# Performance work log

Hardware: AMD Instinct MI355X
Metric: run time of the kernel (lower is better)

Reference implementation:

```python
import jax, jax.numpy as jnp
import numpy as np

EMBED = 768
HIDDEN = 3072
HEADS = 12
EPS = 1e-6


def _ln(x, g, b):
    mu = jnp.mean(x, axis=-1, keepdims=True)
    var = jnp.mean(jnp.square(x - mu), axis=-1, keepdims=True)
    return (x - mu) / jnp.sqrt(var + EPS) * g + b


def setup_inputs() -> dict:
    key = jax.random.key(0)
    ks = jax.random.split(key, 12)
    s = lambda fan_in: 1.0 / np.sqrt(fan_in)
    x = jax.random.normal(ks[0], (16, 1024, EMBED), dtype=jnp.float32)
    return {
        "x": x,
        "ln1_g": jnp.ones((EMBED,), jnp.float32),
        "ln1_b": jnp.zeros((EMBED,), jnp.float32),
        "qkv_w": jax.random.uniform(ks[1], (3 * EMBED, EMBED), jnp.float32, -s(EMBED), s(EMBED)),
        "qkv_b": jax.random.uniform(ks[2], (3 * EMBED,), jnp.float32, -s(EMBED), s(EMBED)),
        "proj_w": jax.random.uniform(ks[3], (EMBED, EMBED), jnp.float32, -s(EMBED), s(EMBED)),
        "proj_b": jax.random.uniform(ks[4], (EMBED,), jnp.float32, -s(EMBED), s(EMBED)),
        "ln2_g": jnp.ones((EMBED,), jnp.float32),
        "ln2_b": jnp.zeros((EMBED,), jnp.float32),
        "fc1_w": jax.random.uniform(ks[5], (HIDDEN, EMBED), jnp.float32, -s(EMBED), s(EMBED)),
        "fc1_b": jax.random.uniform(ks[6], (HIDDEN,), jnp.float32, -s(EMBED), s(EMBED)),
        "fc2_w": jax.random.uniform(ks[7], (EMBED, HIDDEN), jnp.float32, -s(HIDDEN), s(HIDDEN)),
        "fc2_b": jax.random.uniform(ks[8], (EMBED,), jnp.float32, -s(HIDDEN), s(HIDDEN)),
    }


def reference(x, ln1_g, ln1_b, qkv_w, qkv_b, proj_w, proj_b, ln2_g, ln2_b, fc1_w, fc1_b, fc2_w, fc2_b):
    B, N, D = x.shape
    Hd = D // HEADS
    scale = Hd ** -0.5
    # attention branch
    xn = _ln(x, ln1_g, ln1_b)
    qkv = xn @ qkv_w.T + qkv_b  # [B,N,3D]
    qkv = qkv.reshape(B, N, 3, HEADS, Hd).transpose(2, 0, 3, 1, 4)
    q, k, v = qkv[0], qkv[1], qkv[2]  # [B,H,N,Hd]
    attn = jax.nn.softmax(jnp.einsum("bhqd,bhkd->bhqk", q, k) * scale, axis=-1)
    ctx = jnp.einsum("bhqk,bhkd->bhqd", attn, v)
    ctx = ctx.transpose(0, 2, 1, 3).reshape(B, N, D)
    x = x + ctx @ proj_w.T + proj_b
    # MLP branch
    h = _ln(x, ln2_g, ln2_b)
    h = jax.nn.gelu(h @ fc1_w.T + fc1_b, approximate=False)
    x = x + h @ fc2_w.T + fc2_b
    return x
```

## Files before the change

### kernel.cpp

```cpp
#include <hip/hip_runtime.h>
#include <math.h>


typedef unsigned short u16;
typedef __attribute__((ext_vector_type(8))) short bf16x8;
typedef __attribute__((ext_vector_type(4))) float f32x4;

#define MFMA_BF16(a, b, c) __builtin_amdgcn_mfma_f32_16x16x32_bf16((a), (b), (c), 0, 0, 0)
#define MEMFENCE asm volatile("" ::: "memory")
#define WAITV(N) asm volatile("s_waitcnt vmcnt(" #N ")" ::: "memory")
#define WAITLGKM0 asm volatile("s_waitcnt lgkmcnt(0)" ::: "memory")
#define SCHED0 __builtin_amdgcn_sched_barrier(0)

__device__ __forceinline__ float bf2f(u16 v) {
    return __uint_as_float(((unsigned)v) << 16);
}
__device__ __forceinline__ u16 f2bf(float f) {
    unsigned u = __float_as_uint(f);
    u += 0x7fffu + ((u >> 16) & 1u);
    return (u16)(u >> 16);
}

__device__ __forceinline__ float gelu_fast(float v) {
    const float t = v * v;
    const float z = v * (1.5957691216f + 0.0713548162f * t);
    const float e = __expf(-z);
    return v * __builtin_amdgcn_rcpf(1.0f + e);
}

typedef __attribute__((address_space(1))) const void gvoid;
typedef __attribute__((address_space(3))) void lvoid;
__device__ __forceinline__ void gll16(const void* g, void* l) {
    __builtin_amdgcn_global_load_lds((gvoid*)g, (lvoid*)l, 16, 0, 0);
}

__global__ __launch_bounds__(256) void cast32(const float* __restrict__ src,
                                              u16* __restrict__ dst, int n8) {
    const int i = blockIdx.x * 256 + threadIdx.x;
    if (i >= n8) return;
    const float4 a = ((const float4*)src)[2 * i];
    const float4 b = ((const float4*)src)[2 * i + 1];
    bf16x8 r;
    r[0] = (short)f2bf(a.x); r[1] = (short)f2bf(a.y);
    r[2] = (short)f2bf(a.z); r[3] = (short)f2bf(a.w);
    r[4] = (short)f2bf(b.x); r[5] = (short)f2bf(b.y);
    r[6] = (short)f2bf(b.z); r[7] = (short)f2bf(b.w);
    ((bf16x8*)dst)[i] = r;
}

__global__ __launch_bounds__(256) void ln_kernel(const float* __restrict__ x,
                                                 const float* __restrict__ g,
                                                 const float* __restrict__ b,
                                                 u16* __restrict__ out) {
    const int row = blockIdx.x;
    const int t = threadIdx.x;
    const float* xr = x + (size_t)row * 768;
    float v0 = xr[t], v1 = xr[t + 256], v2 = xr[t + 512];
    float s = v0 + v1 + v2;
    float sq = v0 * v0 + v1 * v1 + v2 * v2;
#pragma unroll
    for (int off = 32; off > 0; off >>= 1) {
        s += __shfl_down(s, off);
        sq += __shfl_down(sq, off);
    }
    __shared__ float red_s[4], red_sq[4], sh_mu, sh_rs;
    const int wave = t >> 6, lane = t & 63;
    if (lane == 0) { red_s[wave] = s; red_sq[wave] = sq; }
    __syncthreads();
    if (t == 0) {
        float S = red_s[0] + red_s[1] + red_s[2] + red_s[3];
        float SQ = red_sq[0] + red_sq[1] + red_sq[2] + red_sq[3];
        float mu = S * (1.0f / 768.0f);
        float var = SQ * (1.0f / 768.0f) - mu * mu;
        sh_mu = mu;
        sh_rs = 1.0f / sqrtf(fmaxf(var, 0.0f) + 1e-6f);
    }
    __syncthreads();
    const float mu = sh_mu, rs = sh_rs;
    u16* orow = out + (size_t)row * 768;
    orow[t]       = f2bf((v0 - mu) * rs * g[t]       + b[t]);
    orow[t + 256] = f2bf((v1 - mu) * rs * g[t + 256] + b[t + 256]);
    orow[t + 512] = f2bf((v2 - mu) * rs * g[t + 512] + b[t + 512]);
}

template <int EPI, int BF16B>
__global__ __launch_bounds__(256, 2) void gemm2(
        const u16* __restrict__ A, const void* __restrict__ Bv,
        const float* __restrict__ bias, const float* __restrict__ res,
        void* __restrict__ Cv, u16* __restrict__ vtb, int N, int K) {
    __shared__ __align__(16) u16 As[128 * 32];
    __shared__ __align__(16) u16 Bs[128 * 32];
    const int t = threadIdx.x;
    const int wave = t >> 6, lane = t & 63;
    const int quad = lane >> 4, mr = lane & 15;
    const int wm = wave >> 1, wn = wave & 1;
    const int m0 = blockIdx.y * 128;
    const int n0 = blockIdx.x * 128;

    f32x4 acc[4][4];
#pragma unroll
    for (int i = 0; i < 4; i++)
#pragma unroll
        for (int j = 0; j < 4; j++) acc[i][j] = (f32x4){0.f, 0.f, 0.f, 0.f};

    const int seg = wave * 2;
    const int drow = lane >> 2;
    const int dcol = (lane & 3) * 8;
    const int sr = t >> 2, skv = t & 3;

    for (int k0 = 0; k0 < K; k0 += 32) {
#pragma unroll
        for (int c = 0; c < 2; c++) {
            const int rowA = (seg + c) * 16 + drow;
            gll16(A + (size_t)(m0 + rowA) * K + k0 + dcol, &As[(seg + c) * 512]);
        }
        if (BF16B) {
            const u16* Bh = (const u16*)Bv;
#pragma unroll
            for (int c = 0; c < 2; c++) {
                const int rowB = (seg + c) * 16 + drow;
                gll16(Bh + (size_t)(n0 + rowB) * K + k0 + dcol, &Bs[(seg + c) * 512]);
            }
        } else {
            const float* Bf = (const float*)Bv;
#pragma unroll
            for (int half = 0; half < 2; half++) {
                const float* src = Bf + (size_t)(n0 + sr + half * 64) * K + k0 + skv * 8;
                const float4 a = *(const float4*)src;
                const float4 b2 = *(const float4*)(src + 4);
                bf16x8 r;
                r[0] = (short)f2bf(a.x);  r[1] = (short)f2bf(a.y);
                r[2] = (short)f2bf(a.z);  r[3] = (short)f2bf(a.w);
                r[4] = (short)f2bf(b2.x); r[5] = (short)f2bf(b2.y);
                r[6] = (short)f2bf(b2.z); r[7] = (short)f2bf(b2.w);
                *(bf16x8*)&Bs[(sr + half * 64) * 32 + skv * 8] = r;
            }
        }
        __syncthreads();
        bf16x8 af[4], bfr[4];
#pragma unroll
        for (int i = 0; i < 4; i++)
            af[i] = *(const bf16x8*)&As[(wm * 64 + i * 16 + mr) * 32 + quad * 8];
#pragma unroll
        for (int j = 0; j < 4; j++)
            bfr[j] = *(const bf16x8*)&Bs[(wn * 64 + j * 16 + mr) * 32 + quad * 8];
#pragma unroll
        for (int i = 0; i < 4; i++)
#pragma unroll
            for (int j = 0; j < 4; j++)
                acc[i][j] = MFMA_BF16(af[i], bfr[j], acc[i][j]);
        __syncthreads();
    }

#pragma unroll
    for (int i = 0; i < 4; i++) {
#pragma unroll
        for (int r = 0; r < 4; r++) {
            const int m = m0 + wm * 64 + i * 16 + quad * 4 + r;
#pragma unroll
            for (int j = 0; j < 4; j++) {
                const int n = n0 + wn * 64 + j * 16 + mr;
                float v = acc[i][j][r] + bias[n];
                if (EPI == 1) {
                    v = gelu_fast(v);
                    ((u16*)Cv)[(size_t)m * N + n] = f2bf(v);
                } else if (EPI == 2) {
                    v += res[(size_t)m * N + n];
                    ((float*)Cv)[(size_t)m * N + n] = v;
                } else {
                    if (n < 1536) {
                        const float vq = (n < 768) ? v * 0.125f : v;
                        ((u16*)Cv)[(size_t)m * 1536 + n] = f2bf(vq);
                    } else {
                        const int h = (n - 1536) >> 6, hd = (n - 1536) & 63;
                        const int bb = m >> 10, pos = m & 1023;
                        vtb[((size_t)(bb * 12 + h) * 64 + hd) * 1024 + pos] = f2bf(v);
                    }
                }
            }
        }
    }
}

#define AFRAG(T, ROW, KS) \
    (*(const bf16x8*)&(T)[(ROW)][(((((KS) << 2) | quad)) ^ ((ROW) & 7)) << 3])

template <int EPI>
__global__ __launch_bounds__(512, 2) void gemm8(
        const u16* __restrict__ A, const u16* __restrict__ Bw,
        const float* __restrict__ bias, const float* __restrict__ res,
        void* __restrict__ Cv, u16* __restrict__ vtb, int N, int K) {
    __shared__ __align__(16) u16 SMEM[4][256][64];
    u16(&As)[2][256][64] = *reinterpret_cast<u16(*)[2][256][64]>(&SMEM[0][0][0]);
    u16(&Bs)[2][256][64] = *reinterpret_cast<u16(*)[2][256][64]>(&SMEM[2][0][0]);
    const int t = threadIdx.x;
    const int wave = t >> 6, lane = t & 63;
    const int quad = lane >> 4, mr = lane & 15;
    const int wm = wave >> 2, wn = wave & 3;
    const int gx = gridDim.x;
    const int nwg = gx * gridDim.y;
    int bid = blockIdx.y * gx + blockIdx.x;
    bid = (bid & 7) * (nwg >> 3) + (bid >> 3);
    const int m0 = (bid / gx) * 256, n0 = (bid % gx) * 256;
    const int NT = K >> 6;

    const int srow = wave * 8 + (lane >> 3);
    const int sgrp = ((lane & 7) ^ (lane >> 3)) * 8;

    const u16* Abase = A + (size_t)(m0 + srow) * K + sgrp;
    const u16* Bbase = Bw + (size_t)(n0 + srow) * K + sgrp;

#define STAGE_A(BI, SLOT, KT) \
    gll16(Abase + ((size_t)(SLOT) * 64) * K + (KT) * 64, &As[BI][(SLOT) * 64 + wave * 8][0])
#define STAGE_B(BI, SLOT, KT) \
    gll16(Bbase + ((size_t)(SLOT) * 64) * K + (KT) * 64, &Bs[BI][(SLOT) * 64 + wave * 8][0])

    STAGE_A(0, 0, 0); STAGE_A(0, 2, 0);
    STAGE_B(0, 0, 0); STAGE_B(0, 1, 0);
    STAGE_B(0, 2, 0); STAGE_B(0, 3, 0);
    STAGE_A(0, 1, 0); STAGE_A(0, 3, 0);
    if (NT > 1) { STAGE_A(1, 0, 1); STAGE_A(1, 2, 1); STAGE_B(1, 0, 1); STAGE_B(1, 1, 1); }

    f32x4 acc[8][4];
#pragma unroll
    for (int i = 0; i < 8; i++)
#pragma unroll
        for (int j = 0; j < 4; j++) acc[i][j] = (f32x4){0.f, 0.f, 0.f, 0.f};

    if (NT > 1) { WAITV(6); } else { WAITV(2); }
    __builtin_amdgcn_s_barrier();
    SCHED0;

    for (int kt = 0; kt < NT; ++kt) {
        const int bi = kt & 1;
        const u16(*Ab)[64] = As[bi];
        const u16(*Bb)[64] = Bs[bi];
        const bool st1 = (kt + 1 < NT);
        const bool st2 = (kt + 2 < NT);
        bf16x8 af[4], bfv[4];

#pragma unroll
        for (int i = 0; i < 4; i++) af[i] = AFRAG(Ab, wm * 128 + i * 16 + mr, 0);
#pragma unroll
        for (int j = 0; j < 4; j++) bfv[j] = AFRAG(Bb, wn * 64 + j * 16 + mr, 0);
        if (st1) { STAGE_B(bi ^ 1, 2, kt + 1); STAGE_B(bi ^ 1, 3, kt + 1); }
        SCHED0;
        __builtin_amdgcn_s_barrier();
        WAITLGKM0;
        SCHED0;
        __builtin_amdgcn_s_setprio(1);
#pragma unroll
        for (int i = 0; i < 4; i++)
#pragma unroll
            for (int j = 0; j < 4; j++)
                acc[i][j] = MFMA_BF16(af[i], bfv[j], acc[i][j]);
        __builtin_amdgcn_s_setprio(0);
        SCHED0;
        if (st1) { WAITV(6); } else { WAITV(0); }
        __builtin_amdgcn_s_barrier();
        SCHED0;

#pragma unroll
        for (int i = 0; i < 4; i++) af[i] = AFRAG(Ab, wm * 128 + 64 + i * 16 + mr, 0);
        if (st1) { STAGE_A(bi ^ 1, 1, kt + 1); STAGE_A(bi ^ 1, 3, kt + 1); }
        SCHED0;
        __builtin_amdgcn_s_barrier();
        WAITLGKM0;
        SCHED0;
        __builtin_amdgcn_s_setprio(1);
#pragma unroll
        for (int i = 0; i < 4; i++)
#pragma unroll
            for (int j = 0; j < 4; j++)
                acc[4 + i][j] = MFMA_BF16(af[i], bfv[j], acc[4 + i][j]);
        __builtin_amdgcn_s_setprio(0);
        SCHED0;
        __builtin_amdgcn_s_barrier();
        SCHED0;

#pragma unroll
        for (int i = 0; i < 4; i++) af[i] = AFRAG(Ab, wm * 128 + i * 16 + mr, 1);
#pragma unroll
        for (int j = 0; j < 4; j++) bfv[j] = AFRAG(Bb, wn * 64 + j * 16 + mr, 1);
        SCHED0;
        __builtin_amdgcn_s_barrier();
        WAITLGKM0;
        SCHED0;
        __builtin_amdgcn_s_setprio(1);
#pragma unroll
        for (int i = 0; i < 4; i++)
#pragma unroll
            for (int j = 0; j < 4; j++)
                acc[i][j] = MFMA_BF16(af[i], bfv[j], acc[i][j]);
        __builtin_amdgcn_s_setprio(0);
        SCHED0;
        __builtin_amdgcn_s_barrier();
        SCHED0;

#pragma unroll
        for (int i = 0; i < 4; i++) af[i] = AFRAG(Ab, wm * 128 + 64 + i * 16 + mr, 1);
        if (st2) { STAGE_A(bi, 0, kt + 2); STAGE_A(bi, 2, kt + 2);
                   STAGE_B(bi, 0, kt + 2); STAGE_B(bi, 1, kt + 2); }
        SCHED0;
        __builtin_amdgcn_s_barrier();
        WAITLGKM0;
        SCHED0;
        __builtin_amdgcn_s_setprio(1);
#pragma unroll
        for (int i = 0; i < 4; i++)
#pragma unroll
            for (int j = 0; j < 4; j++)
                acc[4 + i][j] = MFMA_BF16(af[i], bfv[j], acc[4 + i][j]);
        __builtin_amdgcn_s_setprio(0);
        SCHED0;
        if (st2) { WAITV(6); } else if (st1) { WAITV(2); }
        __builtin_amdgcn_s_barrier();
        SCHED0;
    }

    if (EPI == 3 && n0 >= 1536) {
        u16* Ls = &SMEM[0][0][0];
        __syncthreads();
#pragma unroll
        for (int i = 0; i < 8; i++) {
            const int mbase = wm * 128 + i * 16 + quad * 4;
            const int mch = mbase >> 3, mlo = mbase & 7;
#pragma unroll
            for (int j = 0; j < 4; j++) {
                const int nl = wn * 64 + j * 16 + mr;
                float v0 = acc[i][j][0] + bias[n0 + nl];
                float v1 = acc[i][j][1] + bias[n0 + nl];
                float v2 = acc[i][j][2] + bias[n0 + nl];
                float v3 = acc[i][j][3] + bias[n0 + nl];
                ushort4 w;
                w.x = f2bf(v0); w.y = f2bf(v1); w.z = f2bf(v2); w.w = f2bf(v3);
                *(ushort4*)(Ls + nl * 256 + ((mch ^ (nl & 7)) << 3) + mlo) = w;
            }
        }
        __syncthreads();
        const int bb = m0 >> 10, pos0 = m0 & 1023;
#pragma unroll
        for (int it = 0; it < 32; it++) {
            const int nl = it * 8 + wave;
            const int h = (n0 - 1536 + nl) >> 6;
            const int hd = nl & 63;
            const int mch = (lane >> 1) ^ (nl & 7);
            const ushort4 v =
                *(const ushort4*)(Ls + nl * 256 + (mch << 3) + (lane & 1) * 4);
            u16* dst = vtb + ((size_t)(bb * 12 + h) * 64 + hd) * 1024 + pos0 + lane * 4;
            *(ushort4*)dst = v;
        }
    } else {
#pragma unroll
        for (int i = 0; i < 8; i++) {
#pragma unroll
            for (int r = 0; r < 4; r++) {
                const int m = m0 + wm * 128 + i * 16 + quad * 4 + r;
#pragma unroll
                for (int j = 0; j < 4; j++) {
                    const int n = n0 + wn * 64 + j * 16 + mr;
                    float v = acc[i][j][r] + bias[n];
                    if (EPI == 1) {
                        v = gelu_fast(v);
                        ((u16*)Cv)[(size_t)m * N + n] = f2bf(v);
                    } else if (EPI == 2) {
                        v += res[(size_t)m * N + n];
                        ((float*)Cv)[(size_t)m * N + n] = v;
                    } else {
                        const float vq = (n < 768) ? v * 0.125f : v;
                        ((u16*)Cv)[(size_t)m * 1536 + n] = f2bf(vq);
                    }
                }
            }
        }
    }
#undef STAGE_A
#undef STAGE_B
}

__global__ __launch_bounds__(256) void attn2(const u16* __restrict__ qkkb,
                                             const u16* __restrict__ vtb,
                                             u16* __restrict__ ctx) {
    __shared__ __align__(16) u16 Ks[2][64][72];
    __shared__ __align__(16) u16 Vt[2][64][72];
    __shared__ __align__(16) u16 Ps[64][72];
    const int bh = blockIdx.y;
    const int b = bh / 12, h = bh % 12;
    const int q0 = blockIdx.x * 64;
    const int t = threadIdx.x;
    const int wave = t >> 6, lane = t & 63, quad = lane >> 4, mr = lane & 15;

    const u16* qrow = qkkb + (size_t)(b * 1024 + q0 + wave * 16 + mr) * 1536 + h * 64;
    const bf16x8 qf0 = *(const bf16x8*)(qrow + quad * 8);
    const bf16x8 qf1 = *(const bf16x8*)(qrow + 32 + quad * 8);

    const u16* kbase = qkkb + (size_t)b * 1024 * 1536 + 768 + h * 64;
    const u16* vbase = vtb + (size_t)bh * 64 * 1024;

    const int srow = t >> 3;
    const int sv = t & 7;

    f32x4 oacc[4];
#pragma unroll
    for (int j = 0; j < 4; j++) oacc[j] = (f32x4){0.f, 0.f, 0.f, 0.f};
    float lsum[4] = {0.f, 0.f, 0.f, 0.f};

    bf16x8 pk0, pk1, pv0, pv1;
    pk0 = *(const bf16x8*)(kbase + (size_t)(srow)      * 1536 + sv * 8);
    pk1 = *(const bf16x8*)(kbase + (size_t)(srow + 32) * 1536 + sv * 8);
    pv0 = *(const bf16x8*)(vbase + (size_t)(srow)      * 1024 + sv * 8);
    pv1 = *(const bf16x8*)(vbase + (size_t)(srow + 32) * 1024 + sv * 8);
    *(bf16x8*)&Ks[0][srow][sv * 8] = pk0;
    *(bf16x8*)&Ks[0][srow + 32][sv * 8] = pk1;
    *(bf16x8*)&Vt[0][srow][sv * 8] = pv0;
    *(bf16x8*)&Vt[0][srow + 32][sv * 8] = pv1;

    for (int kt = 0; kt < 16; ++kt) {
        __syncthreads();
        const int cur = kt & 1;
        if (kt < 15) {
            const size_t ko = (size_t)(kt + 1) * 64;
            pk0 = *(const bf16x8*)(kbase + (ko + srow)      * 1536 + sv * 8);
            pk1 = *(const bf16x8*)(kbase + (ko + srow + 32) * 1536 + sv * 8);
            pv0 = *(const bf16x8*)(vbase + (size_t)(srow)      * 1024 + ko + sv * 8);
            pv1 = *(const bf16x8*)(vbase + (size_t)(srow + 32) * 1024 + ko + sv * 8);
        }
        f32x4 sf[4];
#pragma unroll
        for (int j = 0; j < 4; j++) {
            const bf16x8 kf0 = *(const bf16x8*)&Ks[cur][j * 16 + mr][quad * 8];
            const bf16x8 kf1 = *(const bf16x8*)&Ks[cur][j * 16 + mr][32 + quad * 8];
            f32x4 s = (f32x4){0.f, 0.f, 0.f, 0.f};
            s = MFMA_BF16(qf0, kf0, s);
            s = MFMA_BF16(qf1, kf1, s);
            sf[j] = s;
        }
#pragma unroll
        for (int r = 0; r < 4; r++) {
            const float p0 = __expf(sf[0][r] - 8.0f);
            const float p1 = __expf(sf[1][r] - 8.0f);
            const float p2 = __expf(sf[2][r] - 8.0f);
            const float p3 = __expf(sf[3][r] - 8.0f);
            lsum[r] += (p0 + p1) + (p2 + p3);
            const int prow = wave * 16 + quad * 4 + r;
            Ps[prow][0 * 16 + mr] = f2bf(p0);
            Ps[prow][1 * 16 + mr] = f2bf(p1);
            Ps[prow][2 * 16 + mr] = f2bf(p2);
            Ps[prow][3 * 16 + mr] = f2bf(p3);
        }
        __asm__ __volatile__("s_waitcnt lgkmcnt(0)" ::: "memory");
#pragma unroll
        for (int st = 0; st < 2; st++) {
            const bf16x8 pf = *(const bf16x8*)&Ps[wave * 16 + mr][st * 32 + quad * 8];
#pragma unroll
            for (int j = 0; j < 4; j++) {
                const bf16x8 vf = *(const bf16x8*)&Vt[cur][j * 16 + mr][st * 32 + quad * 8];
                oacc[j] = MFMA_BF16(pf, vf, oacc[j]);
            }
        }
        if (kt < 15) {
            const int nxt = cur ^ 1;
            *(bf16x8*)&Ks[nxt][srow][sv * 8] = pk0;
            *(bf16x8*)&Ks[nxt][srow + 32][sv * 8] = pk1;
            *(bf16x8*)&Vt[nxt][srow][sv * 8] = pv0;
            *(bf16x8*)&Vt[nxt][srow + 32][sv * 8] = pv1;
        }
    }

#pragma unroll
    for (int r = 0; r < 4; r++) {
#pragma unroll
        for (int off = 1; off < 16; off <<= 1) lsum[r] += __shfl_xor(lsum[r], off);
        const float inv = 1.0f / lsum[r];
        u16* dst = ctx + (size_t)(b * 1024 + q0 + wave * 16 + quad * 4 + r) * 768 + h * 64;
#pragma unroll
        for (int j = 0; j < 4; j++) dst[j * 16 + mr] = f2bf(oacc[j][r] * inv);
    }
}

extern "C" void kernel_launch(void* const* d_in, const int* in_sizes, int n_in,
                              void* d_out, int out_size, void* d_ws, size_t ws_size,
                              hipStream_t stream) {
    const float* x      = (const float*)d_in[0];
    const float* ln1_g  = (const float*)d_in[1];
    const float* ln1_b  = (const float*)d_in[2];
    const float* qkv_w  = (const float*)d_in[3];
    const float* qkv_b  = (const float*)d_in[4];
    const float* proj_w = (const float*)d_in[5];
    const float* proj_b = (const float*)d_in[6];
    const float* ln2_g  = (const float*)d_in[7];
    const float* ln2_b  = (const float*)d_in[8];
    const float* fc1_w  = (const float*)d_in[9];
    const float* fc1_b  = (const float*)d_in[10];
    const float* fc2_w  = (const float*)d_in[11];
    const float* fc2_b  = (const float*)d_in[12];
    float* out = (float*)d_out;

    char* base = (char*)d_ws + 1024;
    u16* xn   = (u16*)base;
    u16* qkkb = (u16*)(base + 25165824);
    u16* vtb  = (u16*)(base + 75497472);
    u16* h1   = (u16*)(base + 25165824);
    u16* ctxb = xn;
    u16* hn   = xn;

    const size_t WOFF = 125830144ull;
    const bool big = ws_size >= 139985920ull;
    u16* wqkv  = (u16*)((char*)d_ws + WOFF);
    u16* wproj = (u16*)((char*)d_ws + WOFF + 3538944);
    u16* wfc1  = (u16*)((char*)d_ws + WOFF + 4718592);
    u16* wfc2  = (u16*)((char*)d_ws + WOFF + 9437184);

    if (big) {
        cast32<<<dim3(864),  dim3(256), 0, stream>>>(qkv_w,  wqkv,  221184);
        cast32<<<dim3(288),  dim3(256), 0, stream>>>(proj_w, wproj, 73728);
        cast32<<<dim3(1152), dim3(256), 0, stream>>>(fc1_w,  wfc1,  294912);
        cast32<<<dim3(1152), dim3(256), 0, stream>>>(fc2_w,  wfc2,  294912);
    }

    ln_kernel<<<dim3(16384), dim3(256), 0, stream>>>(x, ln1_g, ln1_b, xn);

    if (big)
        gemm8<3><<<dim3(9, 64), dim3(512), 0, stream>>>(
            xn, wqkv, qkv_b, nullptr, qkkb, vtb, 2304, 768);
    else
        gemm2<3, 0><<<dim3(18, 128), dim3(256), 0, stream>>>(
            xn, qkv_w, qkv_b, nullptr, qkkb, vtb, 2304, 768);

    attn2<<<dim3(16, 192), dim3(256), 0, stream>>>(qkkb, vtb, ctxb);

    if (big)
        gemm8<2><<<dim3(3, 64), dim3(512), 0, stream>>>(
            ctxb, wproj, proj_b, x, out, nullptr, 768, 768);
    else
        gemm2<2, 0><<<dim3(6, 128), dim3(256), 0, stream>>>(
            ctxb, proj_w, proj_b, x, out, nullptr, 768, 768);

    ln_kernel<<<dim3(16384), dim3(256), 0, stream>>>(out, ln2_g, ln2_b, hn);

    if (big)
        gemm8<1><<<dim3(12, 64), dim3(512), 0, stream>>>(
            hn, wfc1, fc1_b, nullptr, h1, nullptr, 3072, 768);
    else
        gemm2<1, 0><<<dim3(24, 128), dim3(256), 0, stream>>>(
            hn, fc1_w, fc1_b, nullptr, h1, nullptr, 3072, 768);

    if (big)
        gemm8<2><<<dim3(3, 64), dim3(512), 0, stream>>>(
            h1, wfc2, fc2_b, out, out, nullptr, 768, 3072);
    else
        gemm2<2, 0><<<dim3(6, 128), dim3(256), 0, stream>>>(
            h1, fc2_w, fc2_b, out, out, nullptr, 768, 3072);
}
```

Measured before the change: 573.8 us.

## Swap MFMA operands for vectorized GEMM epilogues and remap attention blocks per XCD

For the GELU and residual GEMM epilogues, the MFMA operands are swapped so each lane's accumulator holds four consecutive output columns. This lets bias loads, residual loads and output stores become 4-wide vector accesses instead of scalar strided ones, cutting memory transactions in the fc1 and fc2 epilogues. The attention kernel's block index is remapped so blocks sharing a batch-head land on the same XCD, aiming for better L2 reuse of K and V. The QKV epilogue indexing is rewritten but stays equivalent.

```diff
diff --git a/kernel.cpp b/kernel.cpp
--- a/kernel.cpp
+++ b/kernel.cpp
@@ -185,6 +185,12 @@
 #define AFRAG(T, ROW, KS) \
     (*(const bf16x8*)&(T)[(ROW)][(((((KS) << 2) | quad)) ^ ((ROW) & 7)) << 3])
 
+#define ACCUM(ACCEL, AF, BF)                                  \
+    do {                                                      \
+        if (EPI == 3) (ACCEL) = MFMA_BF16((AF), (BF), (ACCEL)); \
+        else          (ACCEL) = MFMA_BF16((BF), (AF), (ACCEL)); \
+    } while (0)
+
 template <int EPI>
 __global__ __launch_bounds__(512, 2) void gemm8(
         const u16* __restrict__ A, const u16* __restrict__ Bw,
@@ -253,7 +259,7 @@
         for (int i = 0; i < 4; i++)
 #pragma unroll
             for (int j = 0; j < 4; j++)
-                acc[i][j] = MFMA_BF16(af[i], bfv[j], acc[i][j]);
+                ACCUM(acc[i][j], af[i], bfv[j]);
         __builtin_amdgcn_s_setprio(0);
         SCHED0;
         if (st1) { WAITV(6); } else { WAITV(0); }
@@ -272,7 +278,7 @@
         for (int i = 0; i < 4; i++)
 #pragma unroll
             for (int j = 0; j < 4; j++)
-                acc[4 + i][j] = MFMA_BF16(af[i], bfv[j], acc[4 + i][j]);
+                ACCUM(acc[4 + i][j], af[i], bfv[j]);
         __builtin_amdgcn_s_setprio(0);
         SCHED0;
         __builtin_amdgcn_s_barrier();
@@ -291,7 +297,7 @@
         for (int i = 0; i < 4; i++)
 #pragma unroll
             for (int j = 0; j < 4; j++)
-                acc[i][j] = MFMA_BF16(af[i], bfv[j], acc[i][j]);
+                ACCUM(acc[i][j], af[i], bfv[j]);
         __builtin_amdgcn_s_setprio(0);
         SCHED0;
         __builtin_amdgcn_s_barrier();
@@ -310,7 +316,7 @@
         for (int i = 0; i < 4; i++)
 #pragma unroll
             for (int j = 0; j < 4; j++)
-                acc[4 + i][j] = MFMA_BF16(af[i], bfv[j], acc[4 + i][j]);
+                ACCUM(acc[4 + i][j], af[i], bfv[j]);
         __builtin_amdgcn_s_setprio(0);
         SCHED0;
         if (st2) { WAITV(6); } else if (st1) { WAITV(2); }
@@ -318,58 +324,77 @@
         SCHED0;
     }
 
-    if (EPI == 3 && n0 >= 1536) {
-        u16* Ls = &SMEM[0][0][0];
-        __syncthreads();
-#pragma unroll
-        for (int i = 0; i < 8; i++) {
-            const int mbase = wm * 128 + i * 16 + quad * 4;
-            const int mch = mbase >> 3, mlo = mbase & 7;
-#pragma unroll
-            for (int j = 0; j < 4; j++) {
-                const int nl = wn * 64 + j * 16 + mr;
-                float v0 = acc[i][j][0] + bias[n0 + nl];
-                float v1 = acc[i][j][1] + bias[n0 + nl];
-                float v2 = acc[i][j][2] + bias[n0 + nl];
-                float v3 = acc[i][j][3] + bias[n0 + nl];
-                ushort4 w;
-                w.x = f2bf(v0); w.y = f2bf(v1); w.z = f2bf(v2); w.w = f2bf(v3);
-                *(ushort4*)(Ls + nl * 256 + ((mch ^ (nl & 7)) << 3) + mlo) = w;
-            }
-        }
-        __syncthreads();
-        const int bb = m0 >> 10, pos0 = m0 & 1023;
-#pragma unroll
-        for (int it = 0; it < 32; it++) {
-            const int nl = it * 8 + wave;
-            const int h = (n0 - 1536 + nl) >> 6;
-            const int hd = nl & 63;
-            const int mch = (lane >> 1) ^ (nl & 7);
-            const ushort4 v =
-                *(const ushort4*)(Ls + nl * 256 + (mch << 3) + (lane & 1) * 4);
-            u16* dst = vtb + ((size_t)(bb * 12 + h) * 64 + hd) * 1024 + pos0 + lane * 4;
-            *(ushort4*)dst = v;
-        }
-    } else {
-#pragma unroll
-        for (int i = 0; i < 8; i++) {
-#pragma unroll
-            for (int r = 0; r < 4; r++) {
-                const int m = m0 + wm * 128 + i * 16 + quad * 4 + r;
+    if (EPI == 3) {
+        if (n0 >= 1536) {
+            u16* Ls = &SMEM[0][0][0];
+            __syncthreads();
+#pragma unroll
+            for (int i = 0; i < 8; i++) {
+                const int mbase = wm * 128 + i * 16 + quad * 4;
+                const int mch = mbase >> 3, mlo = mbase & 7;
 #pragma unroll
                 for (int j = 0; j < 4; j++) {
-                    const int n = n0 + wn * 64 + j * 16 + mr;
-                    float v = acc[i][j][r] + bias[n];
-                    if (EPI == 1) {
-                        v = gelu_fast(v);
-                        ((u16*)Cv)[(size_t)m * N + n] = f2bf(v);
-                    } else if (EPI == 2) {
-                        v += res[(size_t)m * N + n];
-                        ((float*)Cv)[(size_t)m * N + n] = v;
-                    } else {
+                    const int nl = wn * 64 + j * 16 + mr;
+                    float v0 = acc[i][j][0] + bias[n0 + nl];
+                    float v1 = acc[i][j][1] + bias[n0 + nl];
+                    float v2 = acc[i][j][2] + bias[n0 + nl];
+                    float v3 = acc[i][j][3] + bias[n0 + nl];
+                    ushort4 w;
+                    w.x = f2bf(v0); w.y = f2bf(v1); w.z = f2bf(v2); w.w = f2bf(v3);
+                    *(ushort4*)(Ls + nl * 256 + ((mch ^ (nl & 7)) << 3) + mlo) = w;
+                }
+            }
+            __syncthreads();
+            const int bb = m0 >> 10, pos0 = m0 & 1023;
+#pragma unroll
+            for (int it = 0; it < 32; it++) {
+                const int nl = it * 8 + wave;
+                const int h = (n0 - 1536 + nl) >> 6;
+                const int hd = nl & 63;
+                const int mch = (lane >> 1) ^ (nl & 7);
+                const ushort4 v =
+                    *(const ushort4*)(Ls + nl * 256 + (mch << 3) + (lane & 1) * 4);
+                u16* dst = vtb + ((size_t)(bb * 12 + h) * 64 + hd) * 1024 + pos0 + lane * 4;
+                *(ushort4*)dst = v;
+            }
+        } else {
+#pragma unroll
+            for (int i = 0; i < 8; i++) {
+#pragma unroll
+                for (int r = 0; r < 4; r++) {
+                    const int m = m0 + wm * 128 + (i >> 2) * 64 + (i & 3) * 16 + quad * 4 + r;
+#pragma unroll
+                    for (int j = 0; j < 4; j++) {
+                        const int n = n0 + wn * 64 + j * 16 + mr;
+                        float v = acc[i][j][r] + bias[n];
                         const float vq = (n < 768) ? v * 0.125f : v;
                         ((u16*)Cv)[(size_t)m * 1536 + n] = f2bf(vq);
                     }
+                }
+            }
+        }
+    } else {
+#pragma unroll
+        for (int ii = 0; ii < 8; ii++) {
+            const int m = m0 + wm * 128 + (ii >> 2) * 64 + (ii & 3) * 16 + mr;
+#pragma unroll
+            for (int j = 0; j < 4; j++) {
+                const int n = n0 + wn * 64 + j * 16 + quad * 4;
+                const float4 b4 = *(const float4*)&bias[n];
+                const float v0 = acc[ii][j][0] + b4.x;
+                const float v1 = acc[ii][j][1] + b4.y;
+                const float v2 = acc[ii][j][2] + b4.z;
+                const float v3 = acc[ii][j][3] + b4.w;
+                if (EPI == 1) {
+                    ushort4 w;
+                    w.x = f2bf(gelu_fast(v0)); w.y = f2bf(gelu_fast(v1));
+                    w.z = f2bf(gelu_fast(v2)); w.w = f2bf(gelu_fast(v3));
+                    *(ushort4*)&((u16*)Cv)[(size_t)m * N + n] = w;
+                } else {
+                    const float4 r4 = *(const float4*)&res[(size_t)m * N + n];
+                    float4 o;
+                    o.x = v0 + r4.x; o.y = v1 + r4.y; o.z = v2 + r4.z; o.w = v3 + r4.w;
+                    *(float4*)&((float*)Cv)[(size_t)m * N + n] = o;
                 }
             }
         }
@@ -384,9 +409,11 @@
     __shared__ __align__(16) u16 Ks[2][64][72];
     __shared__ __align__(16) u16 Vt[2][64][72];
     __shared__ __align__(16) u16 Ps[64][72];
-    const int bh = blockIdx.y;
+    const int L = blockIdx.y * gridDim.x + blockIdx.x;
+    const int lxcd = L & 7, li = L >> 3;
+    const int bh = lxcd * 24 + (li >> 4);
+    const int q0 = (li & 15) * 64;
     const int b = bh / 12, h = bh % 12;
-    const int q0 = blockIdx.x * 64;
     const int t = threadIdx.x;
     const int wave = t >> 6, lane = t & 63, quad = lane >> 4, mr = lane & 15;
 
```

After: 585.2 us. No clear change (+2.0%).
